# Optimization experiments

Measured on AMD Instinct MI355X. Metric: run time of the kernel, lower is better.

Reference implementation:

```python
import jax, jax.numpy as jnp
import numpy as np

M_FUZZ = 2.0        # self.m
EPSILON = 1e-8      # self.Epsilon
MAX_ITER = 25       # self.max_iterion


def setup_inputs() -> dict:
    key = jax.random.key(0)
    k1, k2 = jax.random.split(key)
    data = jax.random.normal(k1, (300000, 64), dtype=jnp.float32)
    u0_raw = jax.random.uniform(k2, (300000, 64), dtype=jnp.float32)
    return {"data": data, "u0_raw": u0_raw, "cluster": 64}


def reference(data, u0_raw, cluster):
    # Fuzzy c-means, faithful to GranularComputing.forward:
    #   iterate: C = center(U); U = update(U, C); C_new = center(U);
    #            stop if ||C_new - C||_F < Epsilon; return C (pre-update center).
    m = M_FUZZ
    p = 2.0 / (m - 1.0)  # exponent in membership update (== 2.0)
    N, D = data.shape

    # initialize_matrix_U: random rows normalized to sum to 1
    U0 = u0_raw / jnp.sum(u0_raw, axis=1, keepdims=True)  # [N, c]

    def center(U):
        Um = U ** m                                        # [N, c]
        num = Um.T @ data                                  # [c, D]
        den = jnp.sum(Um, axis=0)[:, None]                 # [c, 1]
        return num / den

    x2 = jnp.sum(data * data, axis=1, keepdims=True)       # [N, 1]

    def sqdist(C):
        # squared Euclidean distances [N, c] via expansion (no N x c x D tensor)
        c2 = jnp.sum(C * C, axis=1)                        # [c]
        return jnp.maximum(x2 + c2 - 2.0 * (data @ C.T), 0.0)

    def step(carry, _):
        U, C_ret, done = carry
        C = center(U)                                      # [c, D]
        # u_ij = 1 / sum_k (d_ij / d_ik)^p  ==  d_ij^{-p} / sum_k d_ik^{-p}
        w = sqdist(C) ** (-p / 2.0)                        # [N, c]
        U_new = w / jnp.sum(w, axis=1, keepdims=True)
        C_new = center(U_new)
        diff = jnp.sqrt(jnp.sum((C_new - C) ** 2))
        # freeze state after convergence (emulates the early break)
        U_out = jnp.where(done, U, U_new)
        C_out = jnp.where(done, C_ret, C)
        return (U_out, C_out, done | (diff < EPSILON)), None

    C0 = jnp.zeros((cluster, D), dtype=data.dtype)
    (_, V, _), _ = jax.lax.scan(
        step, (U0, C0, jnp.array(False)), None, length=MAX_ITER + 1
    )
    return V  # [cluster, D]
```

## Files before the change

kernel.cpp:

```cpp
#include <hip/hip_runtime.h>


#define DM 64
#define CL 64
#define PARTIAL_STRIDE 4160
#define MAX_ITER 25
#define MAX_BLOCKS 1024
#define LDP 72

typedef __attribute__((ext_vector_type(8))) short bf16x8;
typedef __attribute__((ext_vector_type(4))) float f32x4;

__device__ __forceinline__ unsigned f2bf1(float f) {
  unsigned u = __builtin_bit_cast(unsigned, f);
  return (u + 0x7FFFu + ((u >> 16) & 1u)) >> 16;
}
__device__ __forceinline__ unsigned pkbf(float a, float b) {
  return f2bf1(a) | (f2bf1(b) << 16);
}
__device__ __forceinline__ unsigned cvtpk_bf16(float a, float b) {
  unsigned r;
  asm("v_cvt_pk_bf16_f32 %0, %1, %2" : "=v"(r) : "v"(a), "v"(b));
  return r;
}

__device__ __forceinline__ float wave_sum(float v) {
#define DPPADD(ctrl, rmask)                                                  \
  v += __builtin_bit_cast(float, __builtin_amdgcn_update_dpp(                \
           0, __builtin_bit_cast(int, v), ctrl, rmask, 0xf, false));
  DPPADD(0x111, 0xf)
  DPPADD(0x112, 0xf)
  DPPADD(0x114, 0xf)
  DPPADD(0x118, 0xf)
  DPPADD(0x142, 0xa)
  DPPADD(0x143, 0xc)
#undef DPPADD
  return __builtin_bit_cast(
      float, __builtin_amdgcn_readlane(__builtin_bit_cast(int, v), 63));
}

__device__ __forceinline__ float group16_sum(float v) {
#define DPPADD(ctrl)                                                         \
  v += __builtin_bit_cast(float, __builtin_amdgcn_update_dpp(                \
           0, __builtin_bit_cast(int, v), ctrl, 0xf, 0xf, false));
  DPPADD(0xB1)
  DPPADD(0x4E)
  DPPADD(0x141)
  DPPADD(0x140)
#undef DPPADD
  return v;
}

__global__ __launch_bounds__(256)
void fcm_prep(const float* __restrict__ data, float* __restrict__ x2,
              unsigned short* __restrict__ xbf,
              float* __restrict__ diffac, int* __restrict__ done,
              int* __restrict__ ticket, int N) {
  size_t i = (size_t)blockIdx.x * blockDim.x + threadIdx.x;
  if (i == 0) { *diffac = 0.0f; *done = 0; *ticket = 0; }
  size_t nvec = (size_t)N * (DM / 4);
  if (i >= nvec) return;
  float4 v = ((const float4*)data)[i];
  float s = fmaf(v.x, v.x, fmaf(v.y, v.y, fmaf(v.z, v.z, v.w * v.w)));
  float rs = group16_sum(s);
  if ((threadIdx.x & 15) == 0) x2[i >> 4] = rs;
  uint2 pk = {cvtpk_bf16(v.x, v.y), cvtpk_bf16(v.z, v.w)};
  ((uint2*)xbf)[i] = pk;
}

template <bool INIT>
__global__ __launch_bounds__(256, 4)
void fcm_pass(const unsigned short* __restrict__ xbf, const float* __restrict__ x2,
              const float* __restrict__ CU,
              float* __restrict__ partial, const int* __restrict__ done,
              int N, int ntiles) {
  if (!INIT && *done) return;
  __shared__ __align__(16) unsigned short Xb[64 * LDP];
  __shared__ __align__(16) unsigned short XTb[2][64 * LDP];
  __shared__ __align__(16) unsigned short umT[64 * LDP];
  __shared__ __align__(16) float x2s[64];

  const int tid  = threadIdx.x;
  const int w    = __builtin_amdgcn_readfirstlane(tid >> 6);
  const int col  = tid & 15;
  const int quad = (tid >> 4) & 3;

  bf16x8 cf0[4], cf1[4];
  float c2v[4];
  if (!INIT) {
#pragma unroll
    for (int jt = 0; jt < 4; jt++) {
      const float* crow = CU + (size_t)(16 * jt + col) * DM;
      float4 ca = *(const float4*)(crow + quad * 8);
      float4 cb = *(const float4*)(crow + quad * 8 + 4);
      float4 cc = *(const float4*)(crow + 32 + quad * 8);
      float4 cd = *(const float4*)(crow + 32 + quad * 8 + 4);
      float cp = ca.x*ca.x + ca.y*ca.y + ca.z*ca.z + ca.w*ca.w
               + cb.x*cb.x + cb.y*cb.y + cb.z*cb.z + cb.w*cb.w
               + cc.x*cc.x + cc.y*cc.y + cc.z*cc.z + cc.w*cc.w
               + cd.x*cd.x + cd.y*cd.y + cd.z*cd.z + cd.w*cd.w;
      cp += __shfl_xor(cp, 16, 64);
      cp += __shfl_xor(cp, 32, 64);
      c2v[jt] = cp;
      union { bf16x8 v; unsigned u[4]; } P0, P1;
      P0.u[0] = pkbf(ca.x, ca.y); P0.u[1] = pkbf(ca.z, ca.w);
      P0.u[2] = pkbf(cb.x, cb.y); P0.u[3] = pkbf(cb.z, cb.w);
      P1.u[0] = pkbf(cc.x, cc.y); P1.u[1] = pkbf(cc.z, cc.w);
      P1.u[2] = pkbf(cd.x, cd.y); P1.u[3] = pkbf(cd.z, cd.w);
      cf0[jt] = P0.v; cf1[jt] = P1.v;
    }
  }

  union { bf16x8 v; unsigned u[4]; } ON;
  ON.u[0] = ON.u[1] = ON.u[2] = ON.u[3] = 0x3F803F80u;
  const bf16x8 onesf = ON.v;

  f32x4 D2[4];
#pragma unroll
  for (int dt = 0; dt < 4; dt++) D2[dt] = f32x4{0.f, 0.f, 0.f, 0.f};
  f32x4 Dden = f32x4{0.f, 0.f, 0.f, 0.f};

  const int sp  = tid & 63;
  const int sd0 = (tid >> 6) * 8;
  const unsigned short* gsrc = xbf + (size_t)sp * DM + sd0;

  auto do_gemm2 = [&](int cb) {
#pragma unroll
    for (int pb = 0; pb < 2; pb++) {
      bf16x8 au = *(const bf16x8*)(const void*)&umT[(16 * w + col) * LDP + pb * 32 + quad * 8];
      Dden = __builtin_amdgcn_mfma_f32_16x16x32_bf16(au, onesf, Dden, 0, 0, 0);
#pragma unroll
      for (int dt = 0; dt < 4; dt++) {
        bf16x8 bx = *(const bf16x8*)(const void*)&XTb[cb][(dt * 16 + col) * LDP + pb * 32 + quad * 8];
        D2[dt] = __builtin_amdgcn_mfma_f32_16x16x32_bf16(au, bx, D2[dt], 0, 0, 0);
      }
    }
  };

  bf16x8 rv0 = {0, 0, 0, 0, 0, 0, 0, 0};
  bf16x8 rv1 = {0, 0, 0, 0, 0, 0, 0, 0};
  float rx2 = 0.0f;
  {
    int t0 = blockIdx.x;
    if (t0 < ntiles) {
      int base = t0 * 64;
      int np = min(64, N - base);
      if (sp < np) {
        const unsigned short* g = gsrc + (size_t)base * DM;
        rv0 = *(const bf16x8*)(g);
        rv1 = *(const bf16x8*)(g + 32);
      }
      if (tid < 64 && base + tid < N) rx2 = x2[base + tid];
    }
  }

  int c = 0;
  int it = 0;
  for (int t = blockIdx.x; t < ntiles; t += gridDim.x, ++it) {
    const int base = t * 64;
    const int np = min(64, N - base);
    __syncthreads();

    if (it > 0) do_gemm2(c ^ 1);

    *(bf16x8*)(void*)&Xb[sp * LDP + sd0] = rv0;
    *(bf16x8*)(void*)&Xb[sp * LDP + sd0 + 32] = rv1;
#pragma unroll
    for (int k = 0; k < 8; k++) XTb[c][(sd0 + k) * LDP + sp] = (unsigned short)rv0[k];
#pragma unroll
    for (int k = 0; k < 8; k++) XTb[c][(sd0 + 32 + k) * LDP + sp] = (unsigned short)rv1[k];
    if (tid < 64) x2s[tid] = rx2;

    {
      int tn = t + gridDim.x;
      rv0 = bf16x8{0, 0, 0, 0, 0, 0, 0, 0};
      rv1 = bf16x8{0, 0, 0, 0, 0, 0, 0, 0};
      rx2 = 0.0f;
      if (tn < ntiles) {
        int nbase = tn * 64;
        int nnp = min(64, N - nbase);
        if (sp < nnp) {
          const unsigned short* g = gsrc + (size_t)nbase * DM;
          rv0 = *(const bf16x8*)(g);
          rv1 = *(const bf16x8*)(g + 32);
        }
        if (tid < 64 && nbase + tid < N) rx2 = x2[nbase + tid];
      }
    }
    __syncthreads();

    float Wv[4][4];
    if (INIT) {
#pragma unroll
      for (int jt = 0; jt < 4; jt++)
#pragma unroll
        for (int r = 0; r < 4; r++) {
          int pl = 16 * w + quad * 4 + r;
          Wv[jt][r] = (pl < np)
              ? CU[(size_t)(base + pl) * CL + 16 * jt + col] : 0.0f;
        }
    } else {
      bf16x8 a0 = *(const bf16x8*)(const void*)&Xb[(16 * w + col) * LDP + quad * 8];
      bf16x8 a1 = *(const bf16x8*)(const void*)&Xb[(16 * w + col) * LDP + 32 + quad * 8];
      f32x4 x2p = *(const f32x4*)(const void*)&x2s[16 * w + quad * 4];
#pragma unroll
      for (int jt = 0; jt < 4; jt++) {
        f32x4 s = f32x4{0.f, 0.f, 0.f, 0.f};
        s = __builtin_amdgcn_mfma_f32_16x16x32_bf16(a0, cf0[jt], s, 0, 0, 0);
        s = __builtin_amdgcn_mfma_f32_16x16x32_bf16(a1, cf1[jt], s, 0, 0, 0);
#pragma unroll
        for (int r = 0; r < 4; r++) {
          float dist = fmaxf(fmaf(-2.0f, s[r], x2p[r] + c2v[jt]), 0.0f);
          Wv[jt][r] = __builtin_amdgcn_rcpf(dist);
        }
      }
    }

    float rr[4];
#pragma unroll
    for (int r = 0; r < 4; r++) {
      float rs = Wv[0][r] + Wv[1][r] + Wv[2][r] + Wv[3][r];
      rs = group16_sum(rs);
      int pl = 16 * w + quad * 4 + r;
      rr[r] = (pl < np) ? __builtin_amdgcn_rcpf(rs) : 0.0f;
    }

#pragma unroll
    for (int jt = 0; jt < 4; jt++) {
      float u0v = Wv[jt][0] * rr[0], u1v = Wv[jt][1] * rr[1];
      float u2v = Wv[jt][2] * rr[2], u3v = Wv[jt][3] * rr[3];
      uint2 pk = {cvtpk_bf16(u0v * u0v, u1v * u1v),
                  cvtpk_bf16(u2v * u2v, u3v * u3v)};
      *(uint2*)(void*)&umT[(16 * jt + col) * LDP + 16 * w + quad * 4] = pk;
    }
    c ^= 1;
  }

  if (it > 0) {
    __syncthreads();
    do_gemm2(c ^ 1);
  }

  float* pbuf = partial + (size_t)blockIdx.x * PARTIAL_STRIDE;
  if (col == 0) {
    float4 dv = {Dden[0], Dden[1], Dden[2], Dden[3]};
    *(float4*)(void*)&pbuf[CL * DM + 16 * w + quad * 4] = dv;
  }
#pragma unroll
  for (int dt = 0; dt < 4; dt++)
#pragma unroll
    for (int r = 0; r < 4; r++)
      pbuf[(size_t)(16 * w + quad * 4 + r) * DM + dt * 16 + col] = D2[dt][r];
}

__global__ __launch_bounds__(1024, 1)
void fcm_reduce(const float* __restrict__ partial, float* __restrict__ Cnew,
                const float* __restrict__ Cold, float* __restrict__ out,
                float* __restrict__ diffac, int* __restrict__ done,
                int* __restrict__ ticket, int compute_diff, int nb) {
  if (compute_diff && *done) return;
  __shared__ float sm[16 * 64];
  __shared__ float sden[1024];
  __shared__ int lastflag;
  __shared__ float sdiff;
  int j = blockIdx.x;
  int tid = threadIdx.x;
  int d = tid & 63;
  int slice = tid >> 6;
  float s = 0.0f;
  for (int b = slice; b < nb; b += 16)
    s += partial[(size_t)b * PARTIAL_STRIDE + j * DM + d];
  sm[slice * 64 + d] = s;
  float dv = 0.0f;
  for (int b = tid; b < nb; b += 1024)
    dv += partial[(size_t)b * PARTIAL_STRIDE + CL * DM + j];
  sden[tid] = dv;
  __syncthreads();
#pragma unroll
  for (int st = 8; st; st >>= 1) {
    if (slice < st) sm[slice * 64 + d] += sm[(slice + st) * 64 + d];
    __syncthreads();
  }
#pragma unroll
  for (int st = 512; st >= 64; st >>= 1) {
    if (tid < st) sden[tid] += sden[tid + st];
    __syncthreads();
  }
  if (tid < 64) {
    float denj = wave_sum(sden[tid]);
    float c = sm[tid] / denj;
    Cnew[j * DM + tid] = c;
    if (compute_diff) {
      float df = c - Cold[j * DM + tid];
      float tot = wave_sum(df * df);
      if (tid == 0) atomicAdd(diffac, tot);
    }
  }
  if (!compute_diff) return;
  __syncthreads();
  if (tid == 0) {
    __threadfence();
    int t = atomicAdd(ticket, 1);
    lastflag = (t == (int)gridDim.x - 1);
  }
  __syncthreads();
  if (!lastflag) return;
  if (tid == 0) sdiff = atomicAdd(diffac, 0.0f);
  __syncthreads();
  if (sdiff < 1e-16f) {
    for (int i = tid; i < CL * DM; i += 1024) out[i] = Cold[i];
    if (tid == 0) *done = 1;
  }
  if (tid == 0) { *diffac = 0.0f; *ticket = 0; }
}

__global__ void fcm_final(const float* __restrict__ Clast, float* __restrict__ out,
                          const int* __restrict__ done) {
  if (*done) return;
  int i = blockIdx.x * blockDim.x + threadIdx.x;
  if (i < CL * DM) out[i] = Clast[i];
}

extern "C" void kernel_launch(void* const* d_in, const int* in_sizes, int n_in,
                              void* d_out, int out_size, void* d_ws, size_t ws_size,
                              hipStream_t stream) {
  const float* data = (const float*)d_in[0];
  const float* u0   = (const float*)d_in[1];
  float* out = (float*)d_out;
  int N = in_sizes[0] / DM;
  int ntiles = (N + 63) / 64;

  float* ws = (float*)d_ws;
  size_t Noff = ((size_t)N + 15) & ~(size_t)15;
  float* x2 = ws;
  unsigned short* xbf = (unsigned short*)(ws + Noff);
  float* C0 = ws + Noff + (size_t)N * 32;
  float* C1 = C0 + CL * DM;
  float* diffac = C1 + CL * DM;
  int* done = (int*)(diffac + 1);
  int* ticket = (int*)(diffac + 2);
  float* partial = diffac + 16;

  size_t used = Noff + (size_t)N * 32 + 2 * CL * DM + 16;
  size_t avail = (ws_size / 4 > used) ? (ws_size / 4 - used) / PARTIAL_STRIDE : 0;
  int nb = (int)(avail < MAX_BLOCKS ? avail : MAX_BLOCKS);
  if (nb < 1) nb = 1;

  size_t nvec = (size_t)N * (DM / 4);
  hipLaunchKernelGGL(fcm_prep, dim3((unsigned)((nvec + 255) / 256)), dim3(256), 0,
                     stream, data, x2, xbf, diffac, done, ticket, N);
  hipLaunchKernelGGL((fcm_pass<true>), dim3(nb), dim3(256), 0, stream,
                     xbf, x2, u0, partial, done, N, ntiles);
  hipLaunchKernelGGL(fcm_reduce, dim3(64), dim3(1024), 0, stream,
                     partial, C0, C1, out, diffac, done, ticket, 0, nb);

  float* bufs[2] = {C0, C1};
  for (int k = 0; k < MAX_ITER; k++) {
    float* Cc = bufs[k & 1];
    float* Cn = bufs[(k + 1) & 1];
    hipLaunchKernelGGL((fcm_pass<false>), dim3(nb), dim3(256), 0, stream,
                       xbf, x2, Cc, partial, done, N, ntiles);
    hipLaunchKernelGGL(fcm_reduce, dim3(64), dim3(1024), 0, stream,
                       partial, Cn, Cc, out, diffac, done, ticket, 1, nb);
  }
  hipLaunchKernelGGL(fcm_final, dim3(16), dim3(256), 0, stream,
                     bufs[1], out, done);
}
```

Measured before the change: 398.9 us.

## Split GEMM2 across warps by cluster-pair and K-half, reducing via LDS

Each warp now computes two cluster tiles over half of the point (K) dimension instead of one cluster tile over the full K. The four X^T B-fragments are loaded once and reused for both cluster tiles, which cuts LDS reads per MFMA. The two K-halves are combined through shared memory before the partial sums are written. The change also lowers the occupancy hint and MAX_BLOCKS from 4 to 3 blocks per CU and from 1024 to 768 blocks. This gives more registers for the doubled accumulators, at the cost of fewer resident waves and an extra barrier plus LDS round trip at the end.

Measured after the change: 381.7 us. 4.3% less time.

```diff
diff --git a/kernel.cpp b/kernel.cpp
--- a/kernel.cpp
+++ b/kernel.cpp
@@ -5,7 +5,7 @@
 #define CL 64
 #define PARTIAL_STRIDE 4160
 #define MAX_ITER 25
-#define MAX_BLOCKS 1024
+#define MAX_BLOCKS 768
 #define LDP 72
 
 typedef __attribute__((ext_vector_type(8))) short bf16x8;
@@ -69,7 +69,7 @@
 }
 
 template <bool INIT>
-__global__ __launch_bounds__(256, 4)
+__global__ __launch_bounds__(256, 3)
 void fcm_pass(const unsigned short* __restrict__ xbf, const float* __restrict__ x2,
               const float* __restrict__ CU,
               float* __restrict__ partial, const int* __restrict__ done,
@@ -84,6 +84,8 @@
   const int w    = __builtin_amdgcn_readfirstlane(tid >> 6);
   const int col  = tid & 15;
   const int quad = (tid >> 4) & 3;
+  const int jh   = w >> 1;
+  const int kh   = w & 1;
 
   bf16x8 cf0[4], cf1[4];
   float c2v[4];
@@ -115,25 +117,31 @@
   ON.u[0] = ON.u[1] = ON.u[2] = ON.u[3] = 0x3F803F80u;
   const bf16x8 onesf = ON.v;
 
-  f32x4 D2[4];
-#pragma unroll
-  for (int dt = 0; dt < 4; dt++) D2[dt] = f32x4{0.f, 0.f, 0.f, 0.f};
-  f32x4 Dden = f32x4{0.f, 0.f, 0.f, 0.f};
+  f32x4 D2[2][4];
+#pragma unroll
+  for (int jt2 = 0; jt2 < 2; jt2++)
+#pragma unroll
+    for (int dt = 0; dt < 4; dt++) D2[jt2][dt] = f32x4{0.f, 0.f, 0.f, 0.f};
+  f32x4 Dden[2] = {f32x4{0.f, 0.f, 0.f, 0.f}, f32x4{0.f, 0.f, 0.f, 0.f}};
 
   const int sp  = tid & 63;
   const int sd0 = (tid >> 6) * 8;
   const unsigned short* gsrc = xbf + (size_t)sp * DM + sd0;
 
   auto do_gemm2 = [&](int cb) {
-#pragma unroll
-    for (int pb = 0; pb < 2; pb++) {
-      bf16x8 au = *(const bf16x8*)(const void*)&umT[(16 * w + col) * LDP + pb * 32 + quad * 8];
-      Dden = __builtin_amdgcn_mfma_f32_16x16x32_bf16(au, onesf, Dden, 0, 0, 0);
-#pragma unroll
-      for (int dt = 0; dt < 4; dt++) {
-        bf16x8 bx = *(const bf16x8*)(const void*)&XTb[cb][(dt * 16 + col) * LDP + pb * 32 + quad * 8];
-        D2[dt] = __builtin_amdgcn_mfma_f32_16x16x32_bf16(au, bx, D2[dt], 0, 0, 0);
-      }
+    const int kb = kh * 32;
+    bf16x8 bx0 = *(const bf16x8*)(const void*)&XTb[cb][(0 * 16 + col) * LDP + kb + quad * 8];
+    bf16x8 bx1 = *(const bf16x8*)(const void*)&XTb[cb][(1 * 16 + col) * LDP + kb + quad * 8];
+    bf16x8 bx2 = *(const bf16x8*)(const void*)&XTb[cb][(2 * 16 + col) * LDP + kb + quad * 8];
+    bf16x8 bx3 = *(const bf16x8*)(const void*)&XTb[cb][(3 * 16 + col) * LDP + kb + quad * 8];
+#pragma unroll
+    for (int jt2 = 0; jt2 < 2; jt2++) {
+      bf16x8 au = *(const bf16x8*)(const void*)&umT[(16 * (2 * jh + jt2) + col) * LDP + kb + quad * 8];
+      Dden[jt2] = __builtin_amdgcn_mfma_f32_16x16x32_bf16(au, onesf, Dden[jt2], 0, 0, 0);
+      D2[jt2][0] = __builtin_amdgcn_mfma_f32_16x16x32_bf16(au, bx0, D2[jt2][0], 0, 0, 0);
+      D2[jt2][1] = __builtin_amdgcn_mfma_f32_16x16x32_bf16(au, bx1, D2[jt2][1], 0, 0, 0);
+      D2[jt2][2] = __builtin_amdgcn_mfma_f32_16x16x32_bf16(au, bx2, D2[jt2][2], 0, 0, 0);
+      D2[jt2][3] = __builtin_amdgcn_mfma_f32_16x16x32_bf16(au, bx3, D2[jt2][3], 0, 0, 0);
     }
   };
 
@@ -231,7 +239,8 @@
       float u2v = Wv[jt][2] * rr[2], u3v = Wv[jt][3] * rr[3];
       uint2 pk = {cvtpk_bf16(u0v * u0v, u1v * u1v),
                   cvtpk_bf16(u2v * u2v, u3v * u3v)};
-      *(uint2*)(void*)&umT[(16 * jt + col) * LDP + 16 * w + quad * 4] = pk;
+      *(unsigned long long*)(void*)&umT[(16 * jt + col) * LDP + 16 * w + quad * 4] =
+          (unsigned long long)pk.x | ((unsigned long long)pk.y << 32);
     }
     c ^= 1;
   }
@@ -241,16 +250,41 @@
     do_gemm2(c ^ 1);
   }
 
-  float* pbuf = partial + (size_t)blockIdx.x * PARTIAL_STRIDE;
-  if (col == 0) {
-    float4 dv = {Dden[0], Dden[1], Dden[2], Dden[3]};
-    *(float4*)(void*)&pbuf[CL * DM + 16 * w + quad * 4] = dv;
-  }
-#pragma unroll
-  for (int dt = 0; dt < 4; dt++)
-#pragma unroll
-    for (int r = 0; r < 4; r++)
-      pbuf[(size_t)(16 * w + quad * 4 + r) * DM + dt * 16 + col] = D2[dt][r];
+  __syncthreads();
+  float* cmb  = (float*)&XTb[0][0];
+  float* cmbd = (float*)&umT[0];
+  const int lane = tid & 63;
+  if (kh == 1) {
+#pragma unroll
+    for (int jt2 = 0; jt2 < 2; jt2++) {
+#pragma unroll
+      for (int dt = 0; dt < 4; dt++)
+        *(f32x4*)(void*)&cmb[((jh * 64 + lane) * 8 + jt2 * 4 + dt) * 4] = D2[jt2][dt];
+      *(f32x4*)(void*)&cmbd[(jh * 64 + lane) * 8 + jt2 * 4] = Dden[jt2];
+    }
+  }
+  __syncthreads();
+  if (kh == 0) {
+    float* pbuf = partial + (size_t)blockIdx.x * PARTIAL_STRIDE;
+#pragma unroll
+    for (int jt2 = 0; jt2 < 2; jt2++) {
+      const int jt = 2 * jh + jt2;
+#pragma unroll
+      for (int dt = 0; dt < 4; dt++) {
+        f32x4 o = *(const f32x4*)(const void*)&cmb[((jh * 64 + lane) * 8 + jt2 * 4 + dt) * 4];
+        D2[jt2][dt] += o;
+#pragma unroll
+        for (int r = 0; r < 4; r++)
+          pbuf[(size_t)(16 * jt + quad * 4 + r) * DM + dt * 16 + col] = D2[jt2][dt][r];
+      }
+      f32x4 od = *(const f32x4*)(const void*)&cmbd[(jh * 64 + lane) * 8 + jt2 * 4];
+      Dden[jt2] += od;
+      if (col == 0) {
+        float4 dv = {Dden[jt2][0], Dden[jt2][1], Dden[jt2][2], Dden[jt2][3]};
+        *(float4*)(void*)&pbuf[CL * DM + 16 * jt + quad * 4] = dv;
+      }
+    }
+  }
 }
 
 __global__ __launch_bounds__(1024, 1)
```
